# Performance work log

Hardware: AMD Instinct MI355X
Metric: run time of the kernel (lower is better)

Reference implementation:

```python
import jax, jax.numpy as jnp
import numpy as np

H = 400
INP = 3
OUT = 121

def _lstm(x, Wih, Whh, bih, bhh):
    # x: [B,T,D]; Wih: [4H,D]; Whh: [4H,H]; PyTorch gate order i,f,g,o
    B, T, _ = x.shape
    h0 = jnp.zeros((B, H), x.dtype)
    c0 = jnp.zeros((B, H), x.dtype)
    xg = jnp.einsum('btd,gd->btg', x, Wih) + bih + bhh  # [B,T,4H]
    def step(carry, xg_t):
        h, c = carry
        g = xg_t + h @ Whh.T
        i, f, gg, o = jnp.split(g, 4, axis=-1)
        c = jax.nn.sigmoid(f) * c + jax.nn.sigmoid(i) * jnp.tanh(gg)
        h = jax.nn.sigmoid(o) * jnp.tanh(c)
        return (h, c), h
    _, hs = jax.lax.scan(step, (h0, c0), jnp.swapaxes(xg, 0, 1))
    return jnp.swapaxes(hs, 0, 1)  # [B,T,H]


def setup_inputs() -> dict:
    key = jax.random.key(0)
    ks = jax.random.split(key, 16)
    s = 0.05
    d = {
        'X': jax.random.normal(ks[0], (64, 1024, INP), jnp.float32),
        'Wih0': jax.random.normal(ks[1], (4 * H, INP), jnp.float32) * s,
        'Whh0': jax.random.normal(ks[2], (4 * H, H), jnp.float32) * s,
        'bih0': jax.random.normal(ks[3], (4 * H,), jnp.float32) * s,
        'bhh0': jax.random.normal(ks[4], (4 * H,), jnp.float32) * s,
        'Wih1': jax.random.normal(ks[5], (4 * H, INP + H), jnp.float32) * s,
        'Whh1': jax.random.normal(ks[6], (4 * H, H), jnp.float32) * s,
        'bih1': jax.random.normal(ks[7], (4 * H,), jnp.float32) * s,
        'bhh1': jax.random.normal(ks[8], (4 * H,), jnp.float32) * s,
        'Wih2': jax.random.normal(ks[9], (4 * H, INP + H), jnp.float32) * s,
        'Whh2': jax.random.normal(ks[10], (4 * H, H), jnp.float32) * s,
        'bih2': jax.random.normal(ks[11], (4 * H,), jnp.float32) * s,
        'bhh2': jax.random.normal(ks[12], (4 * H,), jnp.float32) * s,
        'Wl': jax.random.normal(ks[13], (OUT, 3 * H), jnp.float32) * s,
        'bl': jax.random.normal(ks[14], (OUT,), jnp.float32) * s,
    }
    return d


def reference(X, Wih0, Whh0, bih0, bhh0, Wih1, Whh1, bih1, bhh1,
              Wih2, Whh2, bih2, bhh2, Wl, bl):
    out1 = _lstm(X, Wih0, Whh0, bih0, bhh0)                              # [B,T,H]
    out2 = _lstm(jnp.concatenate([X, out1], axis=2), Wih1, Whh1, bih1, bhh1)
    out3 = _lstm(jnp.concatenate([X, out2], axis=2), Wih2, Whh2, bih2, bhh2)
    all_outs = jnp.concatenate([out1, out2, out3], axis=2)               # [B,T,3H]
    return jnp.einsum('bth,oh->bto', all_outs, Wl) + bl                  # [B,T,OUT]
```

## Files before the change

kernel.cpp:

```cpp
#include <hip/hip_runtime.h>
#include <hip/hip_bf16.h>

#define H    400
#define SEG  416
#define G4   1600
#define TT   1024
#define BB   64
#define NOUT 121
#define KS0  13
#define KS12 26
#define FPAD 1248
#define KSL  39
#define NG   25

typedef __attribute__((ext_vector_type(8))) short bf16x8;
typedef __attribute__((ext_vector_type(4))) float f32x4;
typedef unsigned short u16;

__device__ __align__(16) u16   g_outs[BB * TT][FPAD];
__device__ __align__(16) u16   g_h[3][2][BB][SEG];
__device__ __align__(16) u16   g_pk0[100][KS0][512];
__device__ __align__(16) u16   g_pk1[100][KS12][512];
__device__ __align__(16) u16   g_pk2[100][KS12][512];
__device__ __align__(16) u16   g_pkl[8][KSL][512];
__device__ float g_bsum[3][G4];
__device__ float g_wx[3][G4][3];
__device__ float g_bl[128];
__device__ __align__(128) int g_f[3][4][32][32];
__device__ __align__(128) int g_fo[2][4][32][32];
__device__ int   g_abort;

__device__ inline u16 f2b(float f) {
  union { float f; unsigned u; } v; v.f = f;
  unsigned r = v.u + 0x7FFF + ((v.u >> 16) & 1);
  return (u16)(r >> 16);
}
__device__ inline float sigm(float x) { return 1.f / (1.f + __expf(-x)); }
__device__ inline float tanh_(float x) { return 2.f * sigm(2.f * x) - 1.f; }

__device__ inline void st16_s(u16* p, unsigned v) {
  asm volatile("global_store_short %0, %1, off sc1" :: "v"(p), "v"(v) : "memory");
}
__device__ inline void st32_s(int* p, int v) {
  asm volatile("global_store_dword %0, %1, off sc1" :: "v"(p), "v"(v) : "memory");
}
__device__ inline int poll_s(const int* p) {
  int v;
  asm volatile("global_load_dword %0, %1, off sc1\n\ts_waitcnt vmcnt(0)"
               : "=v"(v) : "v"(p) : "memory");
  return v;
}
template <int SLEEP>
__device__ inline int wait_line(const int (*line)[32], int tv, int skip) {
  const int slot = threadIdx.x & 31;
  const bool act = (slot < NG) && (slot != skip);
  const int* p = &line[act ? slot : 0][0];
  long n = 0;
  for (;;) {
    int v = poll_s(p);
    if (__all((!act) || (v >= tv))) return 0;
    if (SLEEP) __builtin_amdgcn_s_sleep(2);
    if ((++n & 255) == 0) {
      if (poll_s(&g_abort)) return 1;
      if (n > (1L << 21)) { st32_s(&g_abort, 1); return 1; }
    }
  }
}

__global__ void k_zero() {
  int i = blockIdx.x * blockDim.x + threadIdx.x;
  if (i == 0) g_abort = 0;
  if (i < 3 * 4 * 32 * 32) (&g_f[0][0][0][0])[i] = 0;
  if (i < 2 * 4 * 32 * 32) (&g_fo[0][0][0][0])[i] = 0;
  if (i < 3 * 2 * BB * SEG / 2) ((unsigned*)g_h)[i] = 0u;
  if (i < BB * TT * 24) {
    int r = i / 24, j = i % 24;
    int seg = j >> 3, w = j & 7;
    *(unsigned*)&g_outs[r][seg * SEG + 400 + w * 2] = 0u;
  }
}

__global__ void k_pack_rec(const float* Wih, const float* Whh, int layer,
                           int ksteps, int kin) {
  int i = blockIdx.x * blockDim.x + threadIdx.x;
  int total = 100 * ksteps * 512;
  if (i >= total) return;
  int j = i & 7, lane = (i >> 3) & 63;
  int ks = (i >> 9) % ksteps, nt = (i >> 9) / ksteps;
  int g = nt / 25, jt = nt % 25;
  int n  = g * 400 + jt * 16 + (lane & 15);
  int kk = (lane >> 4) * 8 + j;
  float v = 0.f;
  if (layer == 0) {
    int k = ks * 32 + kk;
    if (k < H) v = Whh[n * H + k];
  } else {
    if (ks < KS0) { int k = ks * 32 + kk;         if (k < H) v = Wih[n * kin + 3 + k]; }
    else          { int k = (ks - KS0) * 32 + kk; if (k < H) v = Whh[n * H + k]; }
  }
  u16* dst = (layer == 0) ? &g_pk0[0][0][0] : (layer == 1 ? &g_pk1[0][0][0] : &g_pk2[0][0][0]);
  dst[i] = f2b(v);
}

__global__ void k_pack_wl(const float* Wl, const float* bl) {
  int i = blockIdx.x * blockDim.x + threadIdx.x;
  if (i < 128) g_bl[i] = (i < NOUT) ? bl[i] : 0.f;
  int total = 8 * KSL * 512;
  if (i >= total) return;
  int j = i & 7, lane = (i >> 3) & 63;
  int ks = (i >> 9) % KSL, nt = (i >> 9) / KSL;
  int n = nt * 16 + (lane & 15);
  int k = ks * 32 + (lane >> 4) * 8 + j;
  int seg = k / SEG, jj = k - seg * SEG;
  float v = 0.f;
  if (n < NOUT && jj < 400) v = Wl[n * 1200 + seg * 400 + jj];
  (&g_pkl[0][0][0])[i] = f2b(v);
}

__global__ void k_pack_misc(const float* Wih0, const float* bih0, const float* bhh0,
                            const float* Wih1, const float* bih1, const float* bhh1,
                            const float* Wih2, const float* bih2, const float* bhh2) {
  int i = blockIdx.x * blockDim.x + threadIdx.x;
  if (i >= 3 * G4) return;
  int l = i / G4, n = i % G4;
  const float* bi = l == 0 ? bih0 : (l == 1 ? bih1 : bih2);
  const float* bh = l == 0 ? bhh0 : (l == 1 ? bhh1 : bhh2);
  const float* wi = l == 0 ? Wih0 : (l == 1 ? Wih1 : Wih2);
  int kin = l == 0 ? 3 : 403;
  g_bsum[l][n] = bi[n] + bh[n];
  for (int c = 0; c < 3; ++c) g_wx[l][n][c] = wi[n * kin + c];
}

__global__ __launch_bounds__(256, 1) void k_lstm(const float* __restrict__ X) {
  const int wg = blockIdx.x;
  int l, w2;
  if (wg < 25)      { l = 0; w2 = wg; }
  else if (wg < 75) { l = 1; w2 = wg - 25; }
  else              { l = 2; w2 = wg - 75; }

  const int tid = threadIdx.x;
  const int lane = tid & 63;
  const int wv = tid >> 6;
  const int brow = lane & 15;
  const int kg = lane >> 4;

  int jt, mtile, kh, pair;
  if (l == 0) { jt = w2; mtile = wv; kh = 1; pair = 0; }
  else { int bg = w2 & 1; jt = w2 >> 1; kh = wv & 1; pair = wv >> 1; mtile = bg * 2 + pair; }
  const int jh = jt * 16 + brow;

  const u16* pk = (l == 0) ? &g_pk0[0][0][0] : (l == 1 ? &g_pk1[0][0][0] : &g_pk2[0][0][0]);
  const int nks = (l == 0) ? KS0 : KS12;
  const int wks0 = (l == 0) ? 0 : kh * 13;

  bf16x8 Bf[4][13];
#pragma unroll
  for (int g = 0; g < 4; ++g)
#pragma unroll
    for (int j = 0; j < 13; ++j)
      Bf[g][j] = *(const bf16x8*)&pk[(((g * 25 + jt) * nks + wks0 + j) * 64 + lane) * 8];

  float bsum[4], wxc[4][3];
#pragma unroll
  for (int g = 0; g < 4; ++g) {
    int n = g * 400 + jh;
    bsum[g] = g_bsum[l][n];
    wxc[g][0] = g_wx[l][n][0];
    wxc[g][1] = g_wx[l][n][1];
    wxc[g][2] = g_wx[l][n][2];
  }
  float cst[4] = {0.f, 0.f, 0.f, 0.f};

  __shared__ float red[2][2][2][64][20];
  __shared__ int s_ab[2][4];

#define GLS(i, OFF) asm volatile("global_load_dwordx4 %0, %1, off offset:" OFF " sc1" \
                                 : "=v"(A[i]) : "v"(rowp))
#define GLS_ALL GLS(0,"0");GLS(1,"64");GLS(2,"128");GLS(3,"192");GLS(4,"256");GLS(5,"320"); \
                GLS(6,"384");GLS(7,"448");GLS(8,"512");GLS(9,"576");GLS(10,"640");          \
                GLS(11,"704");GLS(12,"768")
#define XGATE(xg) { \
  _Pragma("unroll") \
  for (int r = 0; r < 4; ++r) { \
    int row = mtile * 16 + kg * 4 + r; \
    const float* xp = X + ((long)row * TT + t) * 3; \
    float x0 = xp[0], x1 = xp[1], x2 = xp[2]; \
    _Pragma("unroll") \
    for (int g = 0; g < 4; ++g) \
      xg[g][r] = bsum[g] + wxc[g][0] * x0 + wxc[g][1] * x1 + wxc[g][2] * x2; \
  } }
#define MFMA_ALL { asm volatile("s_waitcnt vmcnt(0)" ::: "memory"); \
  __builtin_amdgcn_sched_barrier(0); \
  _Pragma("unroll") \
  for (int j = 0; j < 13; ++j) \
    _Pragma("unroll") \
    for (int g = 0; g < 4; ++g) \
      acc[g] = __builtin_amdgcn_mfma_f32_16x16x32_bf16(A[j], Bf[g][j], acc[g], 0, 0, 0); }

  if (l == 0) {
    for (int t = 0; t < TT; ++t) {
      float xg[4][4];
      XGATE(xg);
      f32x4 acc[4] = {};
      if (t > 0) {
        if (wait_line<0>(g_f[0][mtile], t, jt)) return;
        if (lane == 0) st32_s(&g_fo[0][mtile][jt][0], t);
        const u16* rowp = &g_h[0][(t - 1) & 1][mtile * 16 + brow][kg * 8];
        bf16x8 A[13];
        GLS_ALL;
        MFMA_ALL;
      }
      unsigned hb[4];
#pragma unroll
      for (int r = 0; r < 4; ++r) {
        float gate[4];
#pragma unroll
        for (int g = 0; g < 4; ++g) gate[g] = acc[g][r] + xg[g][r];
        float ig = sigm(gate[0]), fg = sigm(gate[1]);
        float gg = tanh_(gate[2]), og = sigm(gate[3]);
        float c = fg * cst[r] + ig * gg;
        cst[r] = c;
        hb[r] = (unsigned)f2b(og * tanh_(c));
        st16_s(&g_h[0][t & 1][mtile * 16 + kg * 4 + r][jh], hb[r]);
      }
      asm volatile("s_waitcnt vmcnt(0)" ::: "memory");
      if (lane == 0) st32_s(&g_f[0][mtile][jt][0], t + 1);
#pragma unroll
      for (int r = 0; r < 4; ++r)
        st16_s(&g_outs[(long)(mtile * 16 + kg * 4 + r) * TT + t][jh], hb[r]);
    }
    asm volatile("s_waitcnt vmcnt(0)" ::: "memory");
    if (lane == 0) st32_s(&g_fo[0][mtile][jt][0], TT);
    return;
  }

  for (int t = 0; t < TT; ++t) {
    float xg[4][4];
    XGATE(xg);

    int ab = 0;
    f32x4 acc[4] = {};
    if (kh) {
      if (t > 0) {
        ab = wait_line<0>(g_f[l][mtile], t, jt);
        if (!ab) {
          const u16* rowp = &g_h[l][(t - 1) & 1][mtile * 16 + brow][kg * 8];
          bf16x8 A[13];
          GLS_ALL;
          MFMA_ALL;
        }
      }
    } else {
      ab = wait_line<1>(g_fo[l - 1][mtile], t + 1, -1);
      if (!ab) {
        if (l == 1 && t > 0 && lane == 0) st32_s(&g_fo[1][mtile][jt][0], t);
        const u16* rowp = &g_outs[(long)(mtile * 16 + brow) * TT + t][(l - 1) * SEG + kg * 8];
        bf16x8 A[13];
        GLS_ALL;
        MFMA_ALL;
      }
    }
    if (lane == 0) s_ab[t & 1][wv] = ab;

#pragma unroll
    for (int g = 0; g < 4; ++g)
      *(f32x4*)&red[pair][t & 1][kh][lane][g * 4] = acc[g];
    __syncthreads();
    if (s_ab[t & 1][0] | s_ab[t & 1][1] | s_ab[t & 1][2] | s_ab[t & 1][3]) return;
    f32x4 gacc[4];
#pragma unroll
    for (int g = 0; g < 4; ++g)
      gacc[g] = acc[g] + *(const f32x4*)&red[pair][t & 1][kh ^ 1][lane][g * 4];

    unsigned hb[4];
#pragma unroll
    for (int r = 0; r < 4; ++r) {
      float gate[4];
#pragma unroll
      for (int g = 0; g < 4; ++g) gate[g] = gacc[g][r] + xg[g][r];
      float ig = sigm(gate[0]), fg = sigm(gate[1]);
      float gg = tanh_(gate[2]), og = sigm(gate[3]);
      float c = fg * cst[r] + ig * gg;
      cst[r] = c;
      hb[r] = (unsigned)f2b(og * tanh_(c));
    }

    if (kh) {
#pragma unroll
      for (int r = 0; r < 4; ++r)
        st16_s(&g_h[l][t & 1][mtile * 16 + kg * 4 + r][jh], hb[r]);
      asm volatile("s_waitcnt vmcnt(0)" ::: "memory");
      if (lane == 0) st32_s(&g_f[l][mtile][jt][0], t + 1);
    } else {
#pragma unroll
      for (int r = 0; r < 4; ++r)
        st16_s(&g_outs[(long)(mtile * 16 + kg * 4 + r) * TT + t][l * SEG + jh], hb[r]);
    }
  }
  if (!kh && l == 1) {
    asm volatile("s_waitcnt vmcnt(0)" ::: "memory");
    if (lane == 0) st32_s(&g_fo[1][mtile][jt][0], TT);
  }
#undef GLS
#undef GLS_ALL
#undef XGATE
#undef MFMA_ALL
}

__global__ __launch_bounds__(256) void k_final(float* __restrict__ out) {
  int mt   = blockIdx.x * 4 + (threadIdx.x >> 6);
  int lane = threadIdx.x & 63;
  int arow = mt * 16 + (lane & 15);
  int kchunk = (lane >> 4) * 8;
  f32x4 acc[8] = {};
  for (int ks = 0; ks < KSL; ++ks) {
    bf16x8 a = *(const bf16x8*)&g_outs[arow][ks * 32 + kchunk];
#pragma unroll
    for (int nt = 0; nt < 8; ++nt) {
      bf16x8 b = *(const bf16x8*)&g_pkl[nt][ks][lane * 8];
      acc[nt] = __builtin_amdgcn_mfma_f32_16x16x32_bf16(a, b, acc[nt], 0, 0, 0);
    }
  }
#pragma unroll
  for (int nt = 0; nt < 8; ++nt) {
    int o = nt * 16 + (lane & 15);
    if (o >= NOUT) continue;
#pragma unroll
    for (int r = 0; r < 4; ++r) {
      int m = mt * 16 + (lane >> 4) * 4 + r;
      out[(long)m * NOUT + o] = acc[nt][r] + g_bl[o];
    }
  }
}

extern "C" void kernel_launch(void* const* d_in, const int* in_sizes, int n_in,
                              void* d_out, int out_size, void* d_ws, size_t ws_size,
                              hipStream_t stream) {
  const float* X    = (const float*)d_in[0];
  const float* Wih0 = (const float*)d_in[1];
  const float* Whh0 = (const float*)d_in[2];
  const float* bih0 = (const float*)d_in[3];
  const float* bhh0 = (const float*)d_in[4];
  const float* Wih1 = (const float*)d_in[5];
  const float* Whh1 = (const float*)d_in[6];
  const float* bih1 = (const float*)d_in[7];
  const float* bhh1 = (const float*)d_in[8];
  const float* Wih2 = (const float*)d_in[9];
  const float* Whh2 = (const float*)d_in[10];
  const float* bih2 = (const float*)d_in[11];
  const float* bhh2 = (const float*)d_in[12];
  const float* Wl   = (const float*)d_in[13];
  const float* bl   = (const float*)d_in[14];

  k_zero<<<(BB * TT * 24 + 255) / 256, 256, 0, stream>>>();
  k_pack_rec<<<(100 * KS0  * 512 + 255) / 256, 256, 0, stream>>>(nullptr, Whh0, 0, KS0, 3);
  k_pack_rec<<<(100 * KS12 * 512 + 255) / 256, 256, 0, stream>>>(Wih1, Whh1, 1, KS12, 403);
  k_pack_rec<<<(100 * KS12 * 512 + 255) / 256, 256, 0, stream>>>(Wih2, Whh2, 2, KS12, 403);
  k_pack_wl<<<(8 * KSL * 512 + 255) / 256, 256, 0, stream>>>(Wl, bl);
  k_pack_misc<<<(3 * G4 + 255) / 256, 256, 0, stream>>>(Wih0, bih0, bhh0,
                                                        Wih1, bih1, bhh1,
                                                        Wih2, bih2, bhh2);
  k_lstm<<<125, 256, 0, stream>>>(X);
  k_final<<<1024, 256, 0, stream>>>((float*)d_out);
}
```

Before: 4.405 ms.

## Replace flag-plus-data recurrent exchange with self-validating tagged packets

The recurrent hidden-state exchange between workgroups now stores each packet as a 16-byte record carrying the bf16 h values plus the step tag. Consumers poll the data directly and use the tag to check freshness, so the separate flag array, the wait-for-store-then-flag round trip, and the extra reload of h are removed. Consumers restage the data through LDS to form MFMA operands. Separately, the input-side wait prefetches the previous layer's progress flag a step ahead to skip the spin loop when it is already satisfied. The cost is more polling traffic per wait iteration and extra LDS shuffles on both producer and consumer sides.

```diff
diff --git a/kernel.cpp b/kernel.cpp
--- a/kernel.cpp
+++ b/kernel.cpp
@@ -12,13 +12,15 @@
 #define FPAD 1248
 #define KSL  39
 #define NG   25
+#define ALP  424
 
 typedef __attribute__((ext_vector_type(8))) short bf16x8;
 typedef __attribute__((ext_vector_type(4))) float f32x4;
+typedef __attribute__((ext_vector_type(4))) int   i32x4;
 typedef unsigned short u16;
 
 __device__ __align__(16) u16   g_outs[BB * TT][FPAD];
-__device__ __align__(16) u16   g_h[3][2][BB][SEG];
+__device__ __align__(16) int   g_ex[3][4][2][104 * 16 * 4];
 __device__ __align__(16) u16   g_pk0[100][KS0][512];
 __device__ __align__(16) u16   g_pk1[100][KS12][512];
 __device__ __align__(16) u16   g_pk2[100][KS12][512];
@@ -26,7 +28,6 @@
 __device__ float g_bsum[3][G4];
 __device__ float g_wx[3][G4][3];
 __device__ float g_bl[128];
-__device__ __align__(128) int g_f[3][4][32][32];
 __device__ __align__(128) int g_fo[2][4][32][32];
 __device__ int   g_abort;
 
@@ -67,12 +68,73 @@
   }
 }
 
+__device__ __forceinline__ int consume_ex(const char* exl, int tv,
+                                          const bf16x8 Bf[4][13], f32x4 acc[4],
+                                          u16 (*Alw)[ALP], int brow, int kg) {
+  i32x4 va[25];
+  long rounds = 0;
+  for (;;) {
+#define LD4(K, I0) { const char* b = exl + (K) * 4096; \
+    asm volatile("global_load_dwordx4 %0, %4, off sc1\n\t" \
+                 "global_load_dwordx4 %1, %4, off offset:1024 sc1\n\t" \
+                 "global_load_dwordx4 %2, %4, off offset:2048 sc1\n\t" \
+                 "global_load_dwordx4 %3, %4, off offset:3072 sc1" \
+                 : "=v"(va[I0]), "=v"(va[I0+1]), "=v"(va[I0+2]), "=v"(va[I0+3]) \
+                 : "v"(b) : "memory"); }
+    LD4(0, 0) LD4(1, 4) LD4(2, 8) LD4(3, 12) LD4(4, 16) LD4(5, 20)
+#undef LD4
+    { const char* b = exl + 6 * 4096;
+      asm volatile("global_load_dwordx4 %0, %1, off sc1" : "=v"(va[24]) : "v"(b) : "memory"); }
+    asm volatile("s_waitcnt vmcnt(0)" ::: "memory");
+    __builtin_amdgcn_sched_barrier(0);
+    int ok = 1;
+#pragma unroll
+    for (int i = 0; i < 25; ++i) ok &= (va[i][3] == tv);
+    if (__all(ok)) break;
+    if ((++rounds & 31) == 0) {
+      if (poll_s(&g_abort)) return 1;
+      if (rounds > (1L << 15)) { st32_s(&g_abort, 1); return 1; }
+    }
+  }
+#pragma unroll
+  for (int i = 0; i < 25; ++i) {
+    unsigned long long d = (unsigned)va[i][0] | ((unsigned long long)(unsigned)va[i][1] << 32);
+    *(unsigned long long*)&Alw[brow][(i * 4 + kg) * 4] = d;
+  }
+  asm volatile("s_waitcnt lgkmcnt(0)" ::: "memory");
+  __builtin_amdgcn_sched_barrier(0);
+#pragma unroll
+  for (int ks = 0; ks < 13; ++ks) {
+    bf16x8 a = *(const bf16x8*)&Alw[brow][ks * 32 + kg * 8];
+#pragma unroll
+    for (int g = 0; g < 4; ++g)
+      acc[g] = __builtin_amdgcn_mfma_f32_16x16x32_bf16(a, Bf[g][ks], acc[g], 0, 0, 0);
+  }
+  return 0;
+}
+
+__device__ __forceinline__ void produce_ex(int* exb, int jt, int t,
+                                           const unsigned hb[4],
+                                           u16 (*Tw)[20], int lane, int brow, int kg) {
+  Tw[kg * 4 + 0][brow] = (u16)hb[0];
+  Tw[kg * 4 + 1][brow] = (u16)hb[1];
+  Tw[kg * 4 + 2][brow] = (u16)hb[2];
+  Tw[kg * 4 + 3][brow] = (u16)hb[3];
+  asm volatile("s_waitcnt lgkmcnt(0)" ::: "memory");
+  __builtin_amdgcn_sched_barrier(0);
+  const int r = lane & 15, g = lane >> 4;
+  unsigned d0 = *(const unsigned*)&Tw[r][g * 4];
+  unsigned d1 = *(const unsigned*)&Tw[r][g * 4 + 2];
+  i32x4 sv; sv[0] = (int)d0; sv[1] = (int)d1; sv[2] = 0; sv[3] = t + 1;
+  int* ep = exb + ((jt * 4 + g) * 16 + r) * 4;
+  asm volatile("global_store_dwordx4 %0, %1, off sc1" :: "v"(ep), "v"(sv) : "memory");
+}
+
 __global__ void k_zero() {
   int i = blockIdx.x * blockDim.x + threadIdx.x;
   if (i == 0) g_abort = 0;
-  if (i < 3 * 4 * 32 * 32) (&g_f[0][0][0][0])[i] = 0;
   if (i < 2 * 4 * 32 * 32) (&g_fo[0][0][0][0])[i] = 0;
-  if (i < 3 * 2 * BB * SEG / 2) ((unsigned*)g_h)[i] = 0u;
+  if (i < 3 * 4 * 2 * 104 * 16 * 4) (&g_ex[0][0][0][0])[i] = 0;
   if (i < BB * TT * 24) {
     int r = i / 24, j = i % 24;
     int seg = j >> 3, w = j & 7;
@@ -171,8 +233,15 @@
   }
   float cst[4] = {0.f, 0.f, 0.f, 0.f};
 
+  __shared__ __align__(16) u16 Al[4][16][ALP];
+  __shared__ u16 Tt[4][16][20];
   __shared__ float red[2][2][2][64][20];
   __shared__ int s_ab[2][4];
+
+  for (int z = lane; z < 16 * 24; z += 64) Al[wv][z / 24][400 + z % 24] = 0;
+  __syncthreads();
+
+  const int exlo = kg * 256 + brow * 16;
 
 #define GLS(i, OFF) asm volatile("global_load_dwordx4 %0, %1, off offset:" OFF " sc1" \
                                  : "=v"(A[i]) : "v"(rowp))
@@ -203,12 +272,9 @@
       XGATE(xg);
       f32x4 acc[4] = {};
       if (t > 0) {
-        if (wait_line<0>(g_f[0][mtile], t, jt)) return;
+        const char* exl = (const char*)&g_ex[0][mtile][(t - 1) & 1][0] + exlo;
+        if (consume_ex(exl, t, Bf, acc, Al[wv], brow, kg)) return;
         if (lane == 0) st32_s(&g_fo[0][mtile][jt][0], t);
-        const u16* rowp = &g_h[0][(t - 1) & 1][mtile * 16 + brow][kg * 8];
-        bf16x8 A[13];
-        GLS_ALL;
-        MFMA_ALL;
       }
       unsigned hb[4];
 #pragma unroll
@@ -221,10 +287,8 @@
         float c = fg * cst[r] + ig * gg;
         cst[r] = c;
         hb[r] = (unsigned)f2b(og * tanh_(c));
-        st16_s(&g_h[0][t & 1][mtile * 16 + kg * 4 + r][jh], hb[r]);
       }
-      asm volatile("s_waitcnt vmcnt(0)" ::: "memory");
-      if (lane == 0) st32_s(&g_f[0][mtile][jt][0], t + 1);
+      produce_ex(&g_ex[0][mtile][t & 1][0], jt, t, hb, Tt[wv], lane, brow, kg);
 #pragma unroll
       for (int r = 0; r < 4; ++r)
         st16_s(&g_outs[(long)(mtile * 16 + kg * 4 + r) * TT + t][jh], hb[r]);
@@ -233,6 +297,13 @@
     if (lane == 0) st32_s(&g_fo[0][mtile][jt][0], TT);
     return;
   }
+
+  const int slot = lane & 31;
+  const bool act = slot < NG;
+  const int* pp = &g_fo[l - 1][mtile][act ? slot : 0][0];
+  int pvr = 0;
+  if (!kh)
+    asm volatile("global_load_dword %0, %1, off sc1" : "=v"(pvr) : "v"(pp) : "memory");
 
   for (int t = 0; t < TT; ++t) {
     float xg[4][4];
@@ -242,16 +313,15 @@
     f32x4 acc[4] = {};
     if (kh) {
       if (t > 0) {
-        ab = wait_line<0>(g_f[l][mtile], t, jt);
-        if (!ab) {
-          const u16* rowp = &g_h[l][(t - 1) & 1][mtile * 16 + brow][kg * 8];
-          bf16x8 A[13];
-          GLS_ALL;
-          MFMA_ALL;
-        }
+        const char* exl = (const char*)&g_ex[l][mtile][(t - 1) & 1][0] + exlo;
+        ab = consume_ex(exl, t, Bf, acc, Al[wv], brow, kg);
       }
     } else {
-      ab = wait_line<1>(g_fo[l - 1][mtile], t + 1, -1);
+      int pv;
+      asm volatile("s_waitcnt vmcnt(0)\n\tv_mov_b32 %0, %1"
+                   : "=v"(pv) : "v"(pvr) : "memory");
+      if (!__all((!act) || (pv >= t + 1)))
+        ab = wait_line<1>(g_fo[l - 1][mtile], t + 1, -1);
       if (!ab) {
         if (l == 1 && t > 0 && lane == 0) st32_s(&g_fo[1][mtile][jt][0], t);
         const u16* rowp = &g_outs[(long)(mtile * 16 + brow) * TT + t][(l - 1) * SEG + kg * 8];
@@ -286,15 +356,12 @@
     }
 
     if (kh) {
-#pragma unroll
-      for (int r = 0; r < 4; ++r)
-        st16_s(&g_h[l][t & 1][mtile * 16 + kg * 4 + r][jh], hb[r]);
-      asm volatile("s_waitcnt vmcnt(0)" ::: "memory");
-      if (lane == 0) st32_s(&g_f[l][mtile][jt][0], t + 1);
+      produce_ex(&g_ex[l][mtile][t & 1][0], jt, t, hb, Tt[wv], lane, brow, kg);
     } else {
 #pragma unroll
       for (int r = 0; r < 4; ++r)
         st16_s(&g_outs[(long)(mtile * 16 + kg * 4 + r) * TT + t][l * SEG + jh], hb[r]);
+      asm volatile("global_load_dword %0, %1, off sc1" : "=v"(pvr) : "v"(pp) : "memory");
     }
   }
   if (!kh && l == 1) {
```

New measurement: 4.833 ms. +9.7%, slower.
